# Performance work log

Measured on AMD Instinct MI355X. Metric: run time of the kernel, lower is better.

The kernel has to match this reference:

```python
import jax, jax.numpy as jnp
import numpy as np

B, H, S, D = 2, 12, 2048, 64

def setup_inputs() -> dict:
    key = jax.random.key(0)
    kq, kk, kv = jax.random.split(key, 3)
    Q = jax.random.normal(kq, (B, H, S, D), dtype=jnp.float32)
    K = jax.random.normal(kk, (B, H, S, D), dtype=jnp.float32)
    V = jax.random.normal(kv, (B, H, S, D), dtype=jnp.float32)
    return {"Q": Q, "K": K, "V": V}

def reference(Q, K, V):
    # NOTE: original code scales by sqrt(Q.shape[-2]) (the sequence length),
    # not the head dim — reproduced faithfully.
    scale = 1.0 / np.sqrt(Q.shape[-2]).astype(np.float32)
    scores = jnp.einsum('bhqd,bhkd->bhqk', Q, K) * scale  # [B,H,S,S]
    attn = jax.nn.softmax(scores, axis=-1)
    context = jnp.einsum('bhqk,bhkd->bhqd', attn, V)      # [B,H,S,D]
    # torch .squeeze(-1) only removes the last dim if it is size 1; D=64 so no-op
    return context
```

## Files before the change

kernel.cpp:

```cpp
#include <hip/hip_runtime.h>
#include <hip/hip_bf16.h>
#include <math.h>
#include <stdint.h>

#define BATCH 2
#define NH 12
#define SEQ 2048
#define HD 64
#define TQ 64
#define TK 64
#define NHEADS (BATCH*NH)
#define NIT (SEQ / TK)

typedef short bf16x8 __attribute__((ext_vector_type(8)));
typedef float f32x4 __attribute__((ext_vector_type(4)));
typedef float f32x16 __attribute__((ext_vector_type(16)));
typedef unsigned short us4_t __attribute__((ext_vector_type(4)));
typedef unsigned short us8_t __attribute__((ext_vector_type(8)));
typedef unsigned int u32x4 __attribute__((ext_vector_type(4)));

#if __has_builtin(__builtin_amdgcn_exp2f)
#define EXP2F(x) __builtin_amdgcn_exp2f(x)
#else
#define EXP2F(x) exp2f(x)
#endif

static __device__ __forceinline__ unsigned short f2bf(float f) {
    unsigned int u = __float_as_uint(f);
    u += 0x7fffu + ((u >> 16) & 1u);
    return (unsigned short)(u >> 16);
}

static __device__ __forceinline__ unsigned int pack2bf(float a, float b) {
    __hip_bfloat162 v = __float22bfloat162_rn(float2{a, b});
    return *(unsigned int*)&v;
}

static __device__ __forceinline__ int tile_off(int r, int c) {
    int rp  = r >> 1;
    int pos = (((r & 1) << 3) | c) ^ (rp & 15);
    return rp * 128 + pos * 8;
}

__global__ __launch_bounds__(256)
void prep_kv(const float* __restrict__ K, const float* __restrict__ V,
             unsigned short* __restrict__ Kb, unsigned short* __restrict__ Vtb) {
    __shared__ unsigned short T[64][66];
    __shared__ unsigned short KT[4096];
    const int bh   = blockIdx.x >> 5;
    const int tile = blockIdx.x & 31;
    const int s0   = tile * 64;
    const int tid  = threadIdx.x;
    const size_t off = ((size_t)bh * SEQ + s0) * HD;

    #pragma unroll
    for (int u = 0; u < 4; ++u) {
        int idx = u * 1024 + tid * 4;
        int r = idx >> 6, col = idx & 63;
        float4 a = *(const float4*)&K[off + idx];
        uint2 pk = { pack2bf(a.x, a.y), pack2bf(a.z, a.w) };
        *(uint2*)&KT[tile_off(r, col >> 3) + (col & 7)] = pk;
    }
    #pragma unroll
    for (int u = 0; u < 4; ++u) {
        int idx = u * 1024 + tid * 4;
        int r = idx >> 6, col = idx & 63;
        float4 a = *(const float4*)&V[off + idx];
        *(unsigned int*)&T[r][col]     = pack2bf(a.x, a.y);
        *(unsigned int*)&T[r][col + 2] = pack2bf(a.z, a.w);
    }
    __syncthreads();

    {
        const int lane = tid & 63, s = tid >> 6;
        unsigned short* KbT = Kb + ((size_t)(bh * 32 + tile) * 2) * 2048;
        #pragma unroll
        for (int nt = 0; nt < 2; ++nt) {
            bf16x8 f = *(const bf16x8*)&KT[tile_off(nt * 32 + (lane & 31),
                                                    s * 2 + (lane >> 5))];
            *(bf16x8*)&KbT[(size_t)nt * 2048 + s * 512 + lane * 8] = f;
        }
    }
    {
        unsigned short* VbT = Vtb + (size_t)(bh * 32 + tile) * 4096;
        const int g = tid & 7, dd = tid >> 3;
        const int cg = ((g >> 2) * 2 + ((g >> 1) & 1));
        const int hi = g & 1;
        #pragma unroll
        for (int h = 0; h < 2; ++h) {
            int d = dd + 32 * h;
            us8_t r8;
            #pragma unroll
            for (int j = 0; j < 8; ++j) {
                int src = ((g >> 1) << 4) + ((j >> 2) << 3) + ((g & 1) << 2) + (j & 3);
                r8[j] = T[src][d];
            }
            *(us8_t*)&VbT[(size_t)cg * 1024 + hi * 512 + d * 8] = r8;
        }
    }
}

__global__ __launch_bounds__(256, 3)
void fa_main(const float* __restrict__ Q,
             const unsigned short* __restrict__ Kb,
             const unsigned short* __restrict__ Vtb,
             float* __restrict__ O, float qs) {
    const int x  = blockIdx.x & 7;
    const int t  = blockIdx.x >> 3;
    const int bh = x + 8 * (t % 3);
    const int qt = t / 3;
    const int q0 = qt * TQ;

    __shared__ __align__(16) unsigned char SH[16896];
    unsigned short* QS = (unsigned short*)SH;
    float* ORed = (float*)SH;
    float* Lsum = (float*)(SH + 16384);
    float* Linv = (float*)(SH + 16640);

    const int tid  = threadIdx.x;
    const int w    = tid >> 6;
    const int mt   = w >> 1;
    const int nt   = w & 1;
    const int lane = tid & 63;
    const int l31  = lane & 31;
    const int hi   = lane >> 5;

    const float* Qh = Q + ((size_t)bh * SEQ + q0) * HD;

    #pragma unroll
    for (int u = 0; u < 4; ++u) {
        int idx = u * 1024 + tid * 4;
        int r = idx >> 6, col = idx & 63;
        float4 a = *(const float4*)&Qh[idx];
        uint2 pk = { pack2bf(a.x * qs, a.y * qs), pack2bf(a.z * qs, a.w * qs) };
        *(uint2*)&QS[tile_off(r, col >> 3) + (col & 7)] = pk;
    }
    __syncthreads();
    bf16x8 qf[4];
    #pragma unroll
    for (int s = 0; s < 4; ++s)
        qf[s] = *(const bf16x8*)&QS[tile_off(mt * 32 + l31, s * 2 + hi)];
    __syncthreads();

    const unsigned short* kB = Kb  + ((size_t)bh * 32 * 2 + nt) * 2048 + lane * 8;
    const unsigned short* vB = Vtb + (size_t)bh * 32 * 4096
                                   + (size_t)(nt * 2) * 1024 + hi * 512 + l31 * 8;

    f32x16 o[2];
    o[0] = (f32x16)(0.f);
    o[1] = (f32x16)(0.f);
    float lsum = 0.f;

    auto FIN = [&](const f32x16& sp, const bf16x8 (&vp)[2][2]) {
        float e0[8], e1[8];
        #pragma unroll
        for (int r = 0; r < 8; ++r) e0[r] = EXP2F(sp[r]);
        #pragma unroll
        for (int r = 0; r < 8; ++r) e1[r] = EXP2F(sp[8 + r]);
        union { u32x4 d; bf16x8 h; } pu0, pu1;
        pu0.d = (u32x4){ pack2bf(e0[0], e0[1]), pack2bf(e0[2], e0[3]),
                         pack2bf(e0[4], e0[5]), pack2bf(e0[6], e0[7]) };
        pu1.d = (u32x4){ pack2bf(e1[0], e1[1]), pack2bf(e1[2], e1[3]),
                         pack2bf(e1[4], e1[5]), pack2bf(e1[6], e1[7]) };
        bf16x8 pf0 = pu0.h, pf1 = pu1.h;
        __builtin_amdgcn_s_setprio(1);
        o[0] = __builtin_amdgcn_mfma_f32_32x32x16_bf16(pf0, vp[0][0], o[0], 0, 0, 0);
        o[1] = __builtin_amdgcn_mfma_f32_32x32x16_bf16(pf0, vp[1][0], o[1], 0, 0, 0);
        o[0] = __builtin_amdgcn_mfma_f32_32x32x16_bf16(pf1, vp[0][1], o[0], 0, 0, 0);
        o[1] = __builtin_amdgcn_mfma_f32_32x32x16_bf16(pf1, vp[1][1], o[1], 0, 0, 0);
        __builtin_amdgcn_s_setprio(0);
        float t0 = ((e0[0] + e0[1]) + (e0[2] + e0[3]))
                 + ((e0[4] + e0[5]) + (e0[6] + e0[7]));
        float t1 = ((e1[0] + e1[1]) + (e1[2] + e1[3]))
                 + ((e1[4] + e1[5]) + (e1[6] + e1[7]));
        lsum += t0 + t1;
    };

    f32x16 scp;
    bf16x8 vfp[2][2];

    {
        bf16x8 kc[4];
        #pragma unroll
        for (int s = 0; s < 4; ++s) kc[s] = *(const bf16x8*)(kB + s * 512);
        #pragma unroll
        for (int dt = 0; dt < 2; ++dt)
            #pragma unroll
            for (int ks = 0; ks < 2; ++ks)
                vfp[dt][ks] = *(const bf16x8*)(vB + ks * 1024 + dt * 256);
        f32x16 sc = (f32x16)(0.f);
        __builtin_amdgcn_s_setprio(1);
        #pragma unroll
        for (int s = 0; s < 4; ++s)
            sc = __builtin_amdgcn_mfma_f32_32x32x16_bf16(kc[s], qf[s], sc, 0, 0, 0);
        __builtin_amdgcn_s_setprio(0);
        scp = sc;
    }

    #pragma unroll 2
    for (int it = 1; it < NIT; ++it) {
        const unsigned short* kT = kB + (size_t)it * 4096;
        const unsigned short* vT = vB + (size_t)it * 4096;

        bf16x8 vn[2][2];
        #pragma unroll
        for (int dt = 0; dt < 2; ++dt)
            #pragma unroll
            for (int ks = 0; ks < 2; ++ks)
                vn[dt][ks] = *(const bf16x8*)(vT + ks * 1024 + dt * 256);
        bf16x8 kc[4];
        #pragma unroll
        for (int s = 0; s < 4; ++s) kc[s] = *(const bf16x8*)(kT + s * 512);

        FIN(scp, vfp);

        f32x16 scc = (f32x16)(0.f);
        __builtin_amdgcn_s_setprio(1);
        #pragma unroll
        for (int s = 0; s < 4; ++s)
            scc = __builtin_amdgcn_mfma_f32_32x32x16_bf16(kc[s], qf[s], scc, 0, 0, 0);
        __builtin_amdgcn_s_setprio(0);

        scp = scc;
        #pragma unroll
        for (int dt = 0; dt < 2; ++dt)
            #pragma unroll
            for (int ks = 0; ks < 2; ++ks)
                vfp[dt][ks] = vn[dt][ks];
    }

    FIN(scp, vfp);

    lsum += __shfl_xor(lsum, 32, 64);

    if (nt == 1) {
        if (lane < 32) Lsum[mt * 32 + lane] = lsum;
        #pragma unroll
        for (int dt = 0; dt < 2; ++dt) {
            const int d = dt * 32 + l31;
            #pragma unroll
            for (int g = 0; g < 4; ++g) {
                const int m0 = mt * 32 + 8 * g + 4 * hi;
                const int ph = (m0 >> 2) ^ (d & 15);
                float4 v = { o[dt][4*g+0], o[dt][4*g+1], o[dt][4*g+2], o[dt][4*g+3] };
                *(float4*)&ORed[d * 64 + ph * 4] = v;
            }
        }
    }
    __syncthreads();

    if (nt == 0) {
        float ltot = lsum + Lsum[mt * 32 + l31];
        if (lane < 32) Linv[mt * 32 + lane] = 1.0f / ltot;
        float* Oh = O + ((size_t)bh * SEQ + q0) * HD;
        #pragma unroll
        for (int dt = 0; dt < 2; ++dt) {
            const int d = dt * 32 + l31;
            #pragma unroll
            for (int g = 0; g < 4; ++g) {
                const int m0 = mt * 32 + 8 * g + 4 * hi;
                const int ph = (m0 >> 2) ^ (d & 15);
                float4 part = *(const float4*)&ORed[d * 64 + ph * 4];
                float4 inv4 = *(const float4*)&Linv[m0];
                const float* pp = (const float*)&part;
                const float* ii = (const float*)&inv4;
                #pragma unroll
                for (int j = 0; j < 4; ++j)
                    Oh[(size_t)(m0 + j) * HD + d] = (o[dt][4*g+j] + pp[j]) * ii[j];
            }
        }
    }
}

#define PAD 8
#define LSTR (HD + PAD)

__global__ __launch_bounds__(256)
void fa_fwd_fb(const float* __restrict__ Q, const float* __restrict__ K,
               const float* __restrict__ V, float* __restrict__ O) {
    const int x  = blockIdx.x & 7;
    const int t  = blockIdx.x >> 3;
    const int bh = x + 8 * (t % 3);
    const int qt = t / 3;
    const int q0 = qt * TQ;
    const long base = (long)bh * SEQ * HD;

    __shared__ unsigned short Qs[TQ][LSTR];
    __shared__ unsigned short Ks2[64][LSTR];
    __shared__ unsigned short Vt[HD][64 + PAD];
    __shared__ unsigned short Ps2[4][16][LSTR];

    const int tid  = threadIdx.x;
    const int wave = tid >> 6;
    const int lane = tid & 63;
    const int col  = lane & 15;
    const int quad = lane >> 4;
    const int m0   = wave * 16;

    #pragma unroll
    for (int i = 0; i < 4; ++i) {
        int idx = tid + 256 * i;
        int row = idx >> 4;
        int c4  = (idx & 15) * 4;
        float4 v = *(const float4*)&Q[base + (long)(q0 + row) * HD + c4];
        ushort4 b = { f2bf(v.x), f2bf(v.y), f2bf(v.z), f2bf(v.w) };
        *(ushort4*)&Qs[row][c4] = b;
    }
    __syncthreads();

    bf16x8 aq0 = *(const bf16x8*)&Qs[m0 + col][quad * 8];
    bf16x8 aq1 = *(const bf16x8*)&Qs[m0 + col][32 + quad * 8];

    f32x4 o0 = {0.f,0.f,0.f,0.f}, o1 = o0, o2 = o0, o3 = o0;
    float l[4] = {0.f, 0.f, 0.f, 0.f};
    const float scale = 0.022097086912079608f;

    for (int kv0 = 0; kv0 < SEQ; kv0 += 64) {
        __syncthreads();
        #pragma unroll
        for (int i = 0; i < 4; ++i) {
            int idx = tid + 256 * i;
            int row = idx >> 4;
            int c4  = (idx & 15) * 4;
            float4 kv = *(const float4*)&K[base + (long)(kv0 + row) * HD + c4];
            ushort4 kb = { f2bf(kv.x), f2bf(kv.y), f2bf(kv.z), f2bf(kv.w) };
            *(ushort4*)&Ks2[row][c4] = kb;
            float4 vv = *(const float4*)&V[base + (long)(kv0 + row) * HD + c4];
            Vt[c4 + 0][row] = f2bf(vv.x);
            Vt[c4 + 1][row] = f2bf(vv.y);
            Vt[c4 + 2][row] = f2bf(vv.z);
            Vt[c4 + 3][row] = f2bf(vv.w);
        }
        __syncthreads();

        f32x4 sc[4];
        #pragma unroll
        for (int n = 0; n < 4; ++n) {
            bf16x8 b0 = *(const bf16x8*)&Ks2[n * 16 + col][quad * 8];
            bf16x8 b1 = *(const bf16x8*)&Ks2[n * 16 + col][32 + quad * 8];
            f32x4 acc = {0.f,0.f,0.f,0.f};
            acc = __builtin_amdgcn_mfma_f32_16x16x32_bf16(aq0, b0, acc, 0, 0, 0);
            acc = __builtin_amdgcn_mfma_f32_16x16x32_bf16(aq1, b1, acc, 0, 0, 0);
            sc[n] = acc;
        }

        float tsum[4] = {0.f, 0.f, 0.f, 0.f};
        #pragma unroll
        for (int n = 0; n < 4; ++n) {
            #pragma unroll
            for (int r = 0; r < 4; ++r) {
                float p = __expf(sc[n][r] * scale);
                tsum[r] += p;
                Ps2[wave][quad * 4 + r][n * 16 + col] = f2bf(p);
            }
        }
        #pragma unroll
        for (int off = 1; off < 16; off <<= 1) {
            #pragma unroll
            for (int r = 0; r < 4; ++r) tsum[r] += __shfl_xor(tsum[r], off, 64);
        }
        #pragma unroll
        for (int r = 0; r < 4; ++r) l[r] += tsum[r];

        bf16x8 ap0 = *(const bf16x8*)&Ps2[wave][col][quad * 8];
        bf16x8 ap1 = *(const bf16x8*)&Ps2[wave][col][32 + quad * 8];
        #pragma unroll
        for (int n = 0; n < 4; ++n) {
            bf16x8 b0 = *(const bf16x8*)&Vt[n * 16 + col][quad * 8];
            bf16x8 b1 = *(const bf16x8*)&Vt[n * 16 + col][32 + quad * 8];
            f32x4* op = (n == 0) ? &o0 : (n == 1) ? &o1 : (n == 2) ? &o2 : &o3;
            *op = __builtin_amdgcn_mfma_f32_16x16x32_bf16(ap0, b0, *op, 0, 0, 0);
            *op = __builtin_amdgcn_mfma_f32_16x16x32_bf16(ap1, b1, *op, 0, 0, 0);
        }
    }

    float inv[4];
    #pragma unroll
    for (int r = 0; r < 4; ++r) inv[r] = 1.0f / l[r];
    #pragma unroll
    for (int r = 0; r < 4; ++r) {
        long row = base + (long)(q0 + m0 + quad * 4 + r) * HD;
        O[row +  0 + col] = o0[r] * inv[r];
        O[row + 16 + col] = o1[r] * inv[r];
        O[row + 32 + col] = o2[r] * inv[r];
        O[row + 48 + col] = o3[r] * inv[r];
    }
}

extern "C" void kernel_launch(void* const* d_in, const int* in_sizes, int n_in,
                              void* d_out, int out_size, void* d_ws, size_t ws_size,
                              hipStream_t stream) {
    const float* Q = (const float*)d_in[0];
    const float* K = (const float*)d_in[1];
    const float* V = (const float*)d_in[2];
    float* O = (float*)d_out;

    const size_t tensorElems = (size_t)NHEADS * SEQ * HD;
    const size_t need = 2 * tensorElems * sizeof(unsigned short);

    if (ws_size >= need) {
        unsigned short* Kb  = (unsigned short*)d_ws;
        unsigned short* Vtb = Kb + tensorElems;
        const float qs = (float)(1.4426950408889634 / sqrt(2048.0));
        prep_kv<<<dim3(NHEADS * (SEQ / 64)), dim3(256), 0, stream>>>(K, V, Kb, Vtb);
        fa_main<<<dim3(NHEADS * (SEQ / TQ)), dim3(256), 0, stream>>>(Q, Kb, Vtb, O, qs);
    } else {
        fa_fwd_fb<<<dim3(NHEADS * (SEQ / TQ)), dim3(256), 0, stream>>>(Q, K, V, O);
    }
}
```

Before: 115.6 us.

## Prefetch K fragments one tile ahead and coalesce V transpose stores

The main loop now loads K fragments for the next key tile into registers one iteration early, so the QK^T MFMAs use already-resident data and global load latency has a full iteration to hide. The V-transpose prep kernel remaps thread indices so each thread writes a contiguous 16-byte chunk at a linear offset, giving fully coalesced stores. The prefetch raises register pressure (extra K fragments live across FIN) under launch_bounds(256,3), which could cause spills or reduce occupancy.

```diff
diff --git a/kernel.cpp b/kernel.cpp
--- a/kernel.cpp
+++ b/kernel.cpp
@@ -83,19 +83,20 @@
     }
     {
         unsigned short* VbT = Vtb + (size_t)(bh * 32 + tile) * 4096;
-        const int g = tid & 7, dd = tid >> 3;
-        const int cg = ((g >> 2) * 2 + ((g >> 1) & 1));
-        const int hi = g & 1;
         #pragma unroll
         for (int h = 0; h < 2; ++h) {
-            int d = dd + 32 * h;
+            int o8 = tid + 256 * h;
+            int d  = o8 & 63;
+            int hi = (o8 >> 6) & 1;
+            int cg = o8 >> 7;
+            int g  = ((cg >> 1) << 2) | ((cg & 1) << 1) | hi;
             us8_t r8;
             #pragma unroll
             for (int j = 0; j < 8; ++j) {
                 int src = ((g >> 1) << 4) + ((j >> 2) << 3) + ((g & 1) << 2) + (j & 3);
                 r8[j] = T[src][d];
             }
-            *(us8_t*)&VbT[(size_t)cg * 1024 + hi * 512 + d * 8] = r8;
+            *(us8_t*)&VbT[o8 * 8] = r8;
         }
     }
 }
@@ -176,30 +177,35 @@
         lsum += t0 + t1;
     };
 
+    bf16x8 kfc[4];
+    bf16x8 vfp[2][2];
     f32x16 scp;
-    bf16x8 vfp[2][2];
+
+    #pragma unroll
+    for (int s = 0; s < 4; ++s) kfc[s] = *(const bf16x8*)(kB + s * 512);
+    #pragma unroll
+    for (int dt = 0; dt < 2; ++dt)
+        #pragma unroll
+        for (int ks = 0; ks < 2; ++ks)
+            vfp[dt][ks] = *(const bf16x8*)(vB + ks * 1024 + dt * 256);
 
     {
-        bf16x8 kc[4];
-        #pragma unroll
-        for (int s = 0; s < 4; ++s) kc[s] = *(const bf16x8*)(kB + s * 512);
-        #pragma unroll
-        for (int dt = 0; dt < 2; ++dt)
-            #pragma unroll
-            for (int ks = 0; ks < 2; ++ks)
-                vfp[dt][ks] = *(const bf16x8*)(vB + ks * 1024 + dt * 256);
+        bf16x8 kn[4];
+        #pragma unroll
+        for (int s = 0; s < 4; ++s) kn[s] = *(const bf16x8*)(kB + 4096 + s * 512);
         f32x16 sc = (f32x16)(0.f);
         __builtin_amdgcn_s_setprio(1);
         #pragma unroll
         for (int s = 0; s < 4; ++s)
-            sc = __builtin_amdgcn_mfma_f32_32x32x16_bf16(kc[s], qf[s], sc, 0, 0, 0);
+            sc = __builtin_amdgcn_mfma_f32_32x32x16_bf16(kfc[s], qf[s], sc, 0, 0, 0);
         __builtin_amdgcn_s_setprio(0);
         scp = sc;
+        #pragma unroll
+        for (int s = 0; s < 4; ++s) kfc[s] = kn[s];
     }
 
     #pragma unroll 2
     for (int it = 1; it < NIT; ++it) {
-        const unsigned short* kT = kB + (size_t)it * 4096;
         const unsigned short* vT = vB + (size_t)it * 4096;
 
         bf16x8 vn[2][2];
@@ -208,9 +214,12 @@
             #pragma unroll
             for (int ks = 0; ks < 2; ++ks)
                 vn[dt][ks] = *(const bf16x8*)(vT + ks * 1024 + dt * 256);
-        bf16x8 kc[4];
-        #pragma unroll
-        for (int s = 0; s < 4; ++s) kc[s] = *(const bf16x8*)(kT + s * 512);
+        bf16x8 kn[4];
+        if (it + 1 < NIT) {
+            const unsigned short* kT = kB + (size_t)(it + 1) * 4096;
+            #pragma unroll
+            for (int s = 0; s < 4; ++s) kn[s] = *(const bf16x8*)(kT + s * 512);
+        }
 
         FIN(scp, vfp);
 
@@ -218,7 +227,7 @@
         __builtin_amdgcn_s_setprio(1);
         #pragma unroll
         for (int s = 0; s < 4; ++s)
-            scc = __builtin_amdgcn_mfma_f32_32x32x16_bf16(kc[s], qf[s], scc, 0, 0, 0);
+            scc = __builtin_amdgcn_mfma_f32_32x32x16_bf16(kfc[s], qf[s], scc, 0, 0, 0);
         __builtin_amdgcn_s_setprio(0);
 
         scp = scc;
@@ -227,6 +236,10 @@
             #pragma unroll
             for (int ks = 0; ks < 2; ++ks)
                 vfp[dt][ks] = vn[dt][ks];
+        if (it + 1 < NIT) {
+            #pragma unroll
+            for (int s = 0; s < 4; ++s) kfc[s] = kn[s];
+        }
     }
 
     FIN(scp, vfp);
```

Result: no change. 115.2 us (-0.4%).

## Split key range across two blocks per query tile and add reduce kernel

Applied to the files above, without the earlier changes.

Each query tile's key/value iteration is split into two halves processed by separate blocks, doubling the grid and raising the occupancy hint. Unnormalized partial outputs and row sums go to workspace, and a new elementwise kernel sums them and normalizes. The prep kernel's V store indexing is also reorganized for contiguous writes. This trades extra global memory traffic and a third launch for more parallelism and shorter per-block serial loops.

```diff
diff --git a/kernel.cpp b/kernel.cpp
--- a/kernel.cpp
+++ b/kernel.cpp
@@ -11,6 +11,8 @@
 #define TK 64
 #define NHEADS (BATCH*NH)
 #define NIT (SEQ / TK)
+#define NBLK (NHEADS * (SEQ / TQ))
+#define HTILES (NIT / 2)
 
 typedef short bf16x8 __attribute__((ext_vector_type(8)));
 typedef float f32x4 __attribute__((ext_vector_type(4)));
@@ -83,30 +85,34 @@
     }
     {
         unsigned short* VbT = Vtb + (size_t)(bh * 32 + tile) * 4096;
-        const int g = tid & 7, dd = tid >> 3;
-        const int cg = ((g >> 2) * 2 + ((g >> 1) & 1));
-        const int hi = g & 1;
         #pragma unroll
         for (int h = 0; h < 2; ++h) {
-            int d = dd + 32 * h;
+            int o8 = tid + 256 * h;
+            int d  = o8 & 63;
+            int hi = (o8 >> 6) & 1;
+            int cg = o8 >> 7;
+            int g  = ((cg >> 1) << 2) | ((cg & 1) << 1) | hi;
             us8_t r8;
             #pragma unroll
             for (int j = 0; j < 8; ++j) {
                 int src = ((g >> 1) << 4) + ((j >> 2) << 3) + ((g & 1) << 2) + (j & 3);
                 r8[j] = T[src][d];
             }
-            *(us8_t*)&VbT[(size_t)cg * 1024 + hi * 512 + d * 8] = r8;
-        }
-    }
-}
-
-__global__ __launch_bounds__(256, 3)
-void fa_main(const float* __restrict__ Q,
-             const unsigned short* __restrict__ Kb,
-             const unsigned short* __restrict__ Vtb,
-             float* __restrict__ O, float qs) {
-    const int x  = blockIdx.x & 7;
-    const int t  = blockIdx.x >> 3;
+            *(us8_t*)&VbT[o8 * 8] = r8;
+        }
+    }
+}
+
+__global__ __launch_bounds__(256, 6)
+void fa_split(const float* __restrict__ Q,
+              const unsigned short* __restrict__ Kb,
+              const unsigned short* __restrict__ Vtb,
+              float* __restrict__ Opart, float* __restrict__ Lpart, float qs) {
+    const int b    = blockIdx.x;
+    const int half = b & 1;
+    const int bb   = b >> 1;
+    const int x  = bb & 7;
+    const int t  = bb >> 3;
     const int bh = x + 8 * (t % 3);
     const int qt = t / 3;
     const int q0 = qt * TQ;
@@ -115,7 +121,6 @@
     unsigned short* QS = (unsigned short*)SH;
     float* ORed = (float*)SH;
     float* Lsum = (float*)(SH + 16384);
-    float* Linv = (float*)(SH + 16640);
 
     const int tid  = threadIdx.x;
     const int w    = tid >> 6;
@@ -142,9 +147,11 @@
         qf[s] = *(const bf16x8*)&QS[tile_off(mt * 32 + l31, s * 2 + hi)];
     __syncthreads();
 
-    const unsigned short* kB = Kb  + ((size_t)bh * 32 * 2 + nt) * 2048 + lane * 8;
+    const unsigned short* kB = Kb  + ((size_t)bh * 32 * 2 + nt) * 2048 + lane * 8
+                                   + (size_t)half * HTILES * 4096;
     const unsigned short* vB = Vtb + (size_t)bh * 32 * 4096
-                                   + (size_t)(nt * 2) * 1024 + hi * 512 + l31 * 8;
+                                   + (size_t)(nt * 2) * 1024 + hi * 512 + l31 * 8
+                                   + (size_t)half * HTILES * 4096;
 
     f32x16 o[2];
     o[0] = (f32x16)(0.f);
@@ -198,7 +205,7 @@
     }
 
     #pragma unroll 2
-    for (int it = 1; it < NIT; ++it) {
+    for (int it = 1; it < HTILES; ++it) {
         const unsigned short* kT = kB + (size_t)it * 4096;
         const unsigned short* vT = vB + (size_t)it * 4096;
 
@@ -251,8 +258,10 @@
 
     if (nt == 0) {
         float ltot = lsum + Lsum[mt * 32 + l31];
-        if (lane < 32) Linv[mt * 32 + lane] = 1.0f / ltot;
-        float* Oh = O + ((size_t)bh * SEQ + q0) * HD;
+        float* Lp = Lpart + (size_t)half * (NHEADS * SEQ);
+        if (lane < 32) Lp[(size_t)bh * SEQ + q0 + mt * 32 + lane] = ltot;
+        float* Po = Opart + (size_t)half * ((size_t)NHEADS * SEQ * HD)
+                          + ((size_t)bh * SEQ + q0) * HD;
         #pragma unroll
         for (int dt = 0; dt < 2; ++dt) {
             const int d = dt * 32 + l31;
@@ -261,15 +270,26 @@
                 const int m0 = mt * 32 + 8 * g + 4 * hi;
                 const int ph = (m0 >> 2) ^ (d & 15);
                 float4 part = *(const float4*)&ORed[d * 64 + ph * 4];
-                float4 inv4 = *(const float4*)&Linv[m0];
                 const float* pp = (const float*)&part;
-                const float* ii = (const float*)&inv4;
                 #pragma unroll
                 for (int j = 0; j < 4; ++j)
-                    Oh[(size_t)(m0 + j) * HD + d] = (o[dt][4*g+j] + pp[j]) * ii[j];
+                    Po[(size_t)(m0 + j) * HD + d] = o[dt][4*g+j] + pp[j];
             }
         }
     }
+}
+
+__global__ __launch_bounds__(256)
+void reduce_o(const float4* __restrict__ P0, const float4* __restrict__ P1,
+              const float* __restrict__ L0, const float* __restrict__ L1,
+              float4* __restrict__ O) {
+    const int idx = blockIdx.x * 256 + threadIdx.x;
+    const int row = idx >> 4;
+    const float inv = 1.0f / (L0[row] + L1[row]);
+    float4 a = P0[idx], bq = P1[idx];
+    float4 r = { (a.x + bq.x) * inv, (a.y + bq.y) * inv,
+                 (a.z + bq.z) * inv, (a.w + bq.w) * inv };
+    O[idx] = r;
 }
 
 #define PAD 8
@@ -396,14 +416,22 @@
     float* O = (float*)d_out;
 
     const size_t tensorElems = (size_t)NHEADS * SEQ * HD;
-    const size_t need = 2 * tensorElems * sizeof(unsigned short);
+    const size_t lElems      = (size_t)NHEADS * SEQ;
+    const size_t need = 2 * tensorElems * sizeof(unsigned short)
+                      + 2 * tensorElems * sizeof(float)
+                      + 2 * lElems * sizeof(float);
 
     if (ws_size >= need) {
         unsigned short* Kb  = (unsigned short*)d_ws;
         unsigned short* Vtb = Kb + tensorElems;
+        float* Opart = (float*)(Vtb + tensorElems);
+        float* Lpart = Opart + 2 * tensorElems;
         const float qs = (float)(1.4426950408889634 / sqrt(2048.0));
         prep_kv<<<dim3(NHEADS * (SEQ / 64)), dim3(256), 0, stream>>>(K, V, Kb, Vtb);
-        fa_main<<<dim3(NHEADS * (SEQ / TQ)), dim3(256), 0, stream>>>(Q, Kb, Vtb, O, qs);
+        fa_split<<<dim3(2 * NBLK), dim3(256), 0, stream>>>(Q, Kb, Vtb, Opart, Lpart, qs);
+        reduce_o<<<dim3((unsigned)(tensorElems / 4 / 256)), dim3(256), 0, stream>>>(
+            (const float4*)Opart, (const float4*)(Opart + tensorElems),
+            Lpart, Lpart + lElems, (float4*)O);
     } else {
         fa_fwd_fb<<<dim3(NHEADS * (SEQ / TQ)), dim3(256), 0, stream>>>(Q, K, V, O);
     }
```

After: 341.5 us. +195.4%, slower.
